# Performance work log

Measured on AMD Instinct MI355X. Metric: run time of the kernel, lower is better.

## Reference

```python
import jax, jax.numpy as jnp
import numpy as np

N, D_IN = 16384, 1024
E, K = 16, 2
D_EMB, H_UNITS, D_HID = 128, 1024, 512


def setup_inputs() -> dict:
    key = jax.random.key(0)
    ks = jax.random.split(key, 10)
    s = lambda fan_in: 1.0 / np.sqrt(fan_in)
    return {
        "x": jax.random.normal(ks[0], (N, D_IN), jnp.float32),
        "Wr": jax.random.normal(ks[1], (D_IN, D_EMB), jnp.float32) * s(D_IN),
        "br": jnp.zeros((D_EMB,), jnp.float32),
        "expert_embeddings": jax.random.normal(ks[2], (E, D_EMB), jnp.float32) * s(D_EMB),
        "W1": jax.random.normal(ks[3], (E, D_IN, H_UNITS), jnp.float32) * s(D_IN),
        "b1": jnp.zeros((E, H_UNITS), jnp.float32),
        "W2": jax.random.normal(ks[4], (E, H_UNITS, H_UNITS // 2), jnp.float32) * s(H_UNITS),
        "b2": jnp.zeros((E, H_UNITS // 2), jnp.float32),
        "W3": jax.random.normal(ks[5], (E, H_UNITS // 2, D_HID), jnp.float32) * s(H_UNITS // 2),
        "b3": jnp.zeros((E, D_HID), jnp.float32),
    }


def reference(x, Wr, br, expert_embeddings, W1, b1, W2, b2, W3, b3):
    # Router: query per token [N, D_EMB]
    q = x @ Wr + br
    # Negative squared L2 distance to each expert embedding -> scores [N, E]
    d2 = jnp.sum(jnp.square(q[:, None, :] - expert_embeddings[None, :, :]), axis=-1)
    scores = -d2
    # Top-k gating (softmax over the k selected scores only)
    top_k_scores, top_k_idx = jax.lax.top_k(scores, K)        # [N, K]
    gates = jax.nn.softmax(top_k_scores, axis=-1)             # [N, K]
    # Dense all-expert MLP (as the original: every expert on every token)
    h1 = jax.nn.relu(jnp.einsum('nd,edh->enh', x, W1) + b1[:, None, :])   # [E,N,1024]
    h2 = jax.nn.relu(jnp.einsum('enh,ehm->enm', h1, W2) + b2[:, None, :]) # [E,N,512]
    eo = jnp.einsum('enm,emo->eno', h2, W3) + b3[:, None, :]              # [E,N,D_HID]
    eo_t = jnp.transpose(eo, (1, 0, 2))                                   # [N,E,D_HID]
    # Gather top-k expert outputs per token and combine with gates
    sel = jnp.take_along_axis(eo_t, top_k_idx[:, :, None], axis=1)        # [N,K,D_HID]
    combined = jnp.sum(sel * gates[:, :, None], axis=1)                   # [N,D_HID]
    return combined
```

## Files before the change

### kernel.cpp

```cpp
#include <hip/hip_runtime.h>

typedef unsigned short u16;
typedef __attribute__((ext_vector_type(8))) short short8;
typedef __attribute__((ext_vector_type(4))) float f32x4;

#define N_TOK 16384
#define DIN   1024
#define NE    16
#define DEMB  128
#define H1N   1024
#define H2N   512
#define DOUT  512
#define CAP   34816
#define MT    (CAP/128)
#define RBLK  1024

#define OFF_P      0ul
#define OFF_C      65536ul
#define OFF_CTRL   65792ul
#define OFF_E01    66048ul
#define OFF_G01    197120ul
#define OFF_GTOK   328192ul
#define OFF_GGATE  467456ul
#define OFF_TSLOT  606720ul
#define OFF_BH     737792ul
#define OFF_BB     803328ul
#define OFF_W1T    868864ul
#define OFF_W2T    34423296ul
#define OFF_W3T    51200512ul
#define OFF_XBF    59589120ul
#define OFF_H1     93143552ul
#define OFF_H2     164446720ul
#define OFF_EO     OFF_H1

__device__ __forceinline__ u16 f2bf(float f) {
  union { float f; unsigned u; } v; v.f = f;
  unsigned r = v.u + 0x7fff + ((v.u >> 16) & 1);
  return (u16)(r >> 16);
}

__device__ __forceinline__ void async_copy16(const u16* g, u16* l) {
  __builtin_amdgcn_global_load_lds((const __attribute__((address_space(1))) unsigned*)g,
                                   (__attribute__((address_space(3))) unsigned*)l,
                                   16, 0, 0);
}

__global__ void router_prep(const float* __restrict__ Wr, const float* __restrict__ br,
                            const float* __restrict__ emb, float* __restrict__ P,
                            float* __restrict__ c) {
  int idx = blockIdx.x * 256 + threadIdx.x;
  int row = idx >> 4, e = idx & 15;
  float s = 0.f;
  for (int j = 0; j < DEMB; ++j) s += Wr[row * DEMB + j] * emb[e * DEMB + j];
  P[row * NE + e] = 2.f * s;
  if (idx < NE) {
    float cc = 0.f, n2 = 0.f;
    for (int j = 0; j < DEMB; ++j) {
      float ev = emb[idx * DEMB + j];
      cc += br[j] * ev;
      n2 += ev * ev;
    }
    c[idx] = 2.f * cc - n2;
  }
}

__global__ void __launch_bounds__(256) router_score(
    const float* __restrict__ x, const float* __restrict__ P,
    const float* __restrict__ c, int* __restrict__ e01,
    float* __restrict__ g01, int* __restrict__ bhist,
    u16* __restrict__ xbf) {
  __shared__ float xs[16384];
  __shared__ int lh[16];
  int wave = threadIdx.x >> 6, lane = threadIdx.x & 63;
  int e2 = lane & 7, kgl = lane >> 3;
  int tbase = blockIdx.x * 16 + wave * 4;
  float* xw = xs + wave * 4096;

  if (threadIdx.x < 16) lh[threadIdx.x] = 0;

  u16* xbrow = xbf + (size_t)tbase * DIN;
  #pragma unroll
  for (int t = 0; t < 4; ++t) {
    const float* src = x + (size_t)(tbase + t) * DIN;
    #pragma unroll
    for (int q = 0; q < 4; ++q) {
      int g = q * 256 + lane * 4;
      float4 v = *(const float4*)(src + g);
      *(float4*)(xw + t * 1024 + g) = v;
      ushort4 o;
      o.x = f2bf(v.x); o.y = f2bf(v.y); o.z = f2bf(v.z); o.w = f2bf(v.w);
      *(ushort4*)(xbrow + t * DIN + g) = o;
    }
  }
  __syncthreads();

  int te0 = 2 * e2, te1 = te0 + 1;
  float ce0 = c[te0], ce1 = c[te1];
  const float* Pb = P + te0;

  float acc0[4] = {0.f, 0.f, 0.f, 0.f};
  float acc1[4] = {0.f, 0.f, 0.f, 0.f};
  int cbase = kgl * 128;
  #pragma unroll 4
  for (int i = 0; i < 32; ++i) {
    int w = (kgl * 4 + i * 4) & 127;
    int idx = cbase + w;
    float2 pv0 = *(const float2*)(Pb + (size_t)(idx + 0) * NE);
    float2 pv1 = *(const float2*)(Pb + (size_t)(idx + 1) * NE);
    float2 pv2 = *(const float2*)(Pb + (size_t)(idx + 2) * NE);
    float2 pv3 = *(const float2*)(Pb + (size_t)(idx + 3) * NE);
    #pragma unroll
    for (int t = 0; t < 4; ++t) {
      float4 xv = *(const float4*)(xw + t * 1024 + idx);
      acc0[t] = fmaf(xv.x, pv0.x, acc0[t]); acc1[t] = fmaf(xv.x, pv0.y, acc1[t]);
      acc0[t] = fmaf(xv.y, pv1.x, acc0[t]); acc1[t] = fmaf(xv.y, pv1.y, acc1[t]);
      acc0[t] = fmaf(xv.z, pv2.x, acc0[t]); acc1[t] = fmaf(xv.z, pv2.y, acc1[t]);
      acc0[t] = fmaf(xv.w, pv3.x, acc0[t]); acc1[t] = fmaf(xv.w, pv3.y, acc1[t]);
    }
  }

  for (int t = 0; t < 4; ++t) {
    float s0 = acc0[t], s1 = acc1[t];
    #pragma unroll
    for (int off = 8; off <= 32; off <<= 1) {
      s0 += __shfl_xor(s0, off);
      s1 += __shfl_xor(s1, off);
    }
    s0 += ce0; s1 += ce1;
    float hi; int hidx;
    if (s0 >= s1) { hi = s0; hidx = te0; } else { hi = s1; hidx = te1; }
    float m1 = hi; int i1 = hidx;
    #pragma unroll
    for (int off = 1; off < 8; off <<= 1) {
      float so = __shfl_xor(m1, off); int io = __shfl_xor(i1, off);
      if (so > m1 || (so == m1 && io < i1)) { m1 = so; i1 = io; }
    }
    float c2; int c2i;
    if (i1 == te0)      { c2 = s1; c2i = te1; }
    else if (i1 == te1) { c2 = s0; c2i = te0; }
    else                { c2 = hi; c2i = hidx; }
    float m2 = c2; int i2 = c2i;
    #pragma unroll
    for (int off = 1; off < 8; off <<= 1) {
      float so = __shfl_xor(m2, off); int io = __shfl_xor(i2, off);
      if (so > m2 || (so == m2 && io < i2)) { m2 = so; i2 = io; }
    }
    if (lane == 0) {
      int tok = tbase + t;
      float ev = expf(m2 - m1);
      float inv = 1.f / (1.f + ev);
      e01[tok * 2 + 0] = i1; e01[tok * 2 + 1] = i2;
      g01[tok * 2 + 0] = inv; g01[tok * 2 + 1] = ev * inv;
      atomicAdd(&lh[i1], 1);
      atomicAdd(&lh[i2], 1);
    }
  }
  __syncthreads();
  if (threadIdx.x < 16) bhist[blockIdx.x * 16 + threadIdx.x] = lh[threadIdx.x];
}

__global__ void __launch_bounds__(1024) scan_offsets(
    const int* __restrict__ bhist, int* __restrict__ counts,
    int* __restrict__ poff, int* __restrict__ bbase, int* __restrict__ gtok) {
  int t = threadIdx.x;
  int e = t & 15, ch = t >> 4;
  int b0 = ch * 16;
  int s = 0;
  #pragma unroll
  for (int i = 0; i < 16; ++i) s += bhist[(b0 + i) * 16 + e];
  __shared__ int part[64][16];
  __shared__ int chbase[64][16];
  __shared__ int cnt[16];
  __shared__ int pof[16];
  part[ch][e] = s;
  __syncthreads();
  if (t < 16) {
    int run = 0;
    for (int c2 = 0; c2 < 64; ++c2) { chbase[c2][t] = run; run += part[c2][t]; }
    cnt[t] = run;
  }
  __syncthreads();
  if (t == 0) {
    int off = 0;
    for (int e2 = 0; e2 < NE; ++e2) {
      pof[e2] = off;
      poff[e2] = off;
      counts[e2] = cnt[e2];
      off += (cnt[e2] + 127) & ~127;
    }
    poff[NE] = off;
  }
  __syncthreads();
  int padc = ((cnt[e] + 127) & ~127) - cnt[e];
  int pbase = pof[e] + cnt[e];
  if (ch < padc) gtok[pbase + ch] = 0;
  if (ch + 64 < padc) gtok[pbase + ch + 64] = 0;

  int run = pof[e] + chbase[ch][e];
  #pragma unroll
  for (int i = 0; i < 16; ++i) {
    bbase[(b0 + i) * 16 + e] = run;
    run += bhist[(b0 + i) * 16 + e];
  }
}

__global__ void build_lists(const int* __restrict__ e01, const float* __restrict__ g01,
                            const int* __restrict__ bbase, int* __restrict__ gtok,
                            float* __restrict__ ggate, int* __restrict__ tslot) {
  __shared__ int pos[16];
  int tid = threadIdx.x;
  if (tid < 16) pos[tid] = bbase[blockIdx.x * 16 + tid];
  __syncthreads();
  if (tid < 16) {
    int t = blockIdx.x * 16 + tid;
    #pragma unroll
    for (int k = 0; k < 2; ++k) {
      int e = e01[t * 2 + k];
      int p = atomicAdd(&pos[e], 1);
      gtok[p] = t;
      ggate[p] = g01[t * 2 + k];
      tslot[t * 2 + k] = p;
    }
  }
}

template<int K, int N>
__global__ void conv_w(const float* __restrict__ W, u16* __restrict__ WT) {
  __shared__ float tile[64][65];
  int e = blockIdx.z;
  int n0 = blockIdx.x * 64, k0 = blockIdx.y * 64;
  int tx = threadIdx.x & 63, ty = threadIdx.x >> 6;
  const float* Wb = W + (size_t)e * K * N;
  #pragma unroll
  for (int p = 0; p < 16; ++p) {
    int k = p * 4 + ty;
    tile[k][tx] = Wb[(size_t)(k0 + k) * N + n0 + tx];
  }
  __syncthreads();
  u16* WTb = WT + (size_t)e * N * K;
  #pragma unroll
  for (int p = 0; p < 16; ++p) {
    int n = p * 4 + ty;
    WTb[(size_t)(n0 + n) * K + k0 + tx] = f2bf(tile[tx][n]);
  }
}

template<int MODE, bool INDIR>
__global__ void __launch_bounds__(256)
gemm_moe(const u16* __restrict__ A, const u16* __restrict__ Ball,
         const float* __restrict__ bias, u16* __restrict__ Cb, float* __restrict__ outF,
         const int* __restrict__ poff, const int* __restrict__ counts,
         const int* __restrict__ gtok, const float* __restrict__ ggate,
         int K, int N, int nblk) {
  __shared__ u16 Asm[2][4096];
  __shared__ u16 Bsm[2][4096];

  int bid = blockIdx.x;
  int q = nblk >> 3, r = nblk & 7;
  int xcd = bid & 7, sidx = bid >> 3;
  int wg = (xcd < r ? xcd * (q + 1) : r * (q + 1) + (xcd - r) * q) + sidx;
  int NB = N >> 7;
  int rb = wg / NB, nb = wg - rb * NB;

  int row_base = rb * 128;
  if (row_base >= poff[NE]) return;
  int e = 0;
  while (row_base >= poff[e + 1]) ++e;

  int tid = threadIdx.x;
  int wave = tid >> 6, lane = tid & 63;
  int wm = wave >> 1, wn = wave & 1;
  int fr = lane & 15, kq = lane >> 4;
  int n_base = nb * 128;

  const u16* Brow = Ball + (size_t)e * N * K + (size_t)n_base * K;

  int rr0 = tid >> 2, rr1 = rr0 + 64;
  int ch8 = ((tid & 3) ^ ((rr0 >> 1) & 3)) * 8;
  const u16 *a0, *a1;
  if constexpr (INDIR) {
    a0 = A + (size_t)gtok[row_base + rr0] * K;
    a1 = A + (size_t)gtok[row_base + rr1] * K;
  } else {
    a0 = A + (size_t)(row_base + rr0) * K;
    a1 = A + (size_t)(row_base + rr1) * K;
  }
  const u16* b0 = Brow + (size_t)rr0 * K;
  const u16* b1 = Brow + (size_t)rr1 * K;

  f32x4 acc[4][4];
  #pragma unroll
  for (int m = 0; m < 4; ++m)
    #pragma unroll
    for (int n = 0; n < 4; ++n)
      acc[m][n] = (f32x4){0.f, 0.f, 0.f, 0.f};

  int swz = (fr >> 1) & 3;

  auto stage_tile = [&](int buf, int kt) {
    async_copy16(a0 + kt + ch8, &Asm[buf][tid * 8]);
    async_copy16(a1 + kt + ch8, &Asm[buf][(256 + tid) * 8]);
    async_copy16(b0 + kt + ch8, &Bsm[buf][tid * 8]);
    async_copy16(b1 + kt + ch8, &Bsm[buf][(256 + tid) * 8]);
  };

  stage_tile(0, 0);
  __syncthreads();

  int nstep = K >> 5;
  int cur = 0;
  for (int s = 0; s < nstep; ++s) {
    if (s + 1 < nstep) stage_tile(cur ^ 1, (s + 1) << 5);
    short8 av[4], bv[4];
    #pragma unroll
    for (int m = 0; m < 4; ++m)
      av[m] = *(const short8*)(&Asm[cur][((wm * 64 + m * 16 + fr) * 4 + (kq ^ swz)) * 8]);
    #pragma unroll
    for (int n = 0; n < 4; ++n)
      bv[n] = *(const short8*)(&Bsm[cur][((wn * 64 + n * 16 + fr) * 4 + (kq ^ swz)) * 8]);
    #pragma unroll
    for (int m = 0; m < 4; ++m)
      #pragma unroll
      for (int n = 0; n < 4; ++n)
        acc[m][n] = __builtin_amdgcn_mfma_f32_16x16x32_bf16(av[m], bv[n], acc[m][n], 0, 0, 0);
    __syncthreads();
    cur ^= 1;
  }

  int crow = (lane >> 4) * 4;
  int ccol = lane & 15;
  const float* be = bias + (size_t)e * N;
  if constexpr (MODE == 0) {
    #pragma unroll
    for (int m = 0; m < 4; ++m) {
      int gr0 = row_base + wm * 64 + m * 16 + crow;
      #pragma unroll
      for (int n = 0; n < 4; ++n) {
        int gc = n_base + wn * 64 + n * 16 + ccol;
        float bvs = be[gc];
        #pragma unroll
        for (int r2 = 0; r2 < 4; ++r2) {
          float v = acc[m][n][r2] + bvs;
          v = v > 0.f ? v : 0.f;
          Cb[(size_t)(gr0 + r2) * N + gc] = f2bf(v);
        }
      }
    }
  } else {
    #pragma unroll
    for (int m = 0; m < 4; ++m) {
      int gr0 = row_base + wm * 64 + m * 16 + crow;
      #pragma unroll
      for (int n = 0; n < 4; ++n) {
        int gc = n_base + wn * 64 + n * 16 + ccol;
        float bvs = be[gc];
        #pragma unroll
        for (int r2 = 0; r2 < 4; ++r2)
          outF[(size_t)(gr0 + r2) * N + gc] = acc[m][n][r2] + bvs;
      }
    }
  }
}

__global__ void __launch_bounds__(256) combine_out(
    const float* __restrict__ eo, const int* __restrict__ tslot,
    const float* __restrict__ g01, float* __restrict__ out) {
  int wave = threadIdx.x >> 6, lane = threadIdx.x & 63;
  int tok = blockIdx.x * 4 + wave;
  int s0 = tslot[tok * 2 + 0], s1 = tslot[tok * 2 + 1];
  float g0 = g01[tok * 2 + 0], g1 = g01[tok * 2 + 1];
  const float* r0 = eo + (size_t)s0 * DOUT + lane * 8;
  const float* r1 = eo + (size_t)s1 * DOUT + lane * 8;
  float* o = out + (size_t)tok * DOUT + lane * 8;
  #pragma unroll
  for (int j = 0; j < 2; ++j) {
    float4 v0 = ((const float4*)r0)[j];
    float4 v1 = ((const float4*)r1)[j];
    float4 ov;
    ov.x = g0 * v0.x + g1 * v1.x;
    ov.y = g0 * v0.y + g1 * v1.y;
    ov.z = g0 * v0.z + g1 * v1.z;
    ov.w = g0 * v0.w + g1 * v1.w;
    ((float4*)o)[j] = ov;
  }
}

extern "C" void kernel_launch(void* const* d_in, const int* in_sizes, int n_in,
                              void* d_out, int out_size, void* d_ws, size_t ws_size,
                              hipStream_t stream) {
  const float* x   = (const float*)d_in[0];
  const float* Wr  = (const float*)d_in[1];
  const float* br  = (const float*)d_in[2];
  const float* emb = (const float*)d_in[3];
  const float* W1  = (const float*)d_in[4];
  const float* b1  = (const float*)d_in[5];
  const float* W2  = (const float*)d_in[6];
  const float* b2  = (const float*)d_in[7];
  const float* W3  = (const float*)d_in[8];
  const float* b3  = (const float*)d_in[9];
  float* out = (float*)d_out;
  char* ws = (char*)d_ws;

  float* P      = (float*)(ws + OFF_P);
  float* c      = (float*)(ws + OFF_C);
  int*   counts = (int*)(ws + OFF_CTRL);
  int*   poff   = (int*)(ws + OFF_CTRL + 128);
  int*   e01    = (int*)(ws + OFF_E01);
  float* g01    = (float*)(ws + OFF_G01);
  int*   gtok   = (int*)(ws + OFF_GTOK);
  float* ggate  = (float*)(ws + OFF_GGATE);
  int*   tslot  = (int*)(ws + OFF_TSLOT);
  int*   bhist  = (int*)(ws + OFF_BH);
  int*   bbase  = (int*)(ws + OFF_BB);
  u16*   W1T    = (u16*)(ws + OFF_W1T);
  u16*   W2T    = (u16*)(ws + OFF_W2T);
  u16*   W3T    = (u16*)(ws + OFF_W3T);
  u16*   xbf    = (u16*)(ws + OFF_XBF);
  u16*   h1     = (u16*)(ws + OFF_H1);
  u16*   h2     = (u16*)(ws + OFF_H2);
  float* eo     = (float*)(ws + OFF_EO);

  conv_w<DIN, H1N><<<dim3(H1N / 64, DIN / 64, NE), 256, 0, stream>>>(W1, W1T);
  conv_w<H1N, H2N><<<dim3(H2N / 64, H1N / 64, NE), 256, 0, stream>>>(W2, W2T);
  conv_w<H2N, DOUT><<<dim3(DOUT / 64, H2N / 64, NE), 256, 0, stream>>>(W3, W3T);

  router_prep<<<64, 256, 0, stream>>>(Wr, br, emb, P, c);
  router_score<<<RBLK, 256, 0, stream>>>(x, P, c, e01, g01, bhist, xbf);
  scan_offsets<<<1, 1024, 0, stream>>>(bhist, counts, poff, bbase, gtok);
  build_lists<<<RBLK, 64, 0, stream>>>(e01, g01, bbase, gtok, ggate, tslot);

  int nb1 = (H1N / 128) * MT;
  int nb2 = (H2N / 128) * MT;
  int nb3 = (DOUT / 128) * MT;
  gemm_moe<0, true><<<nb1, 256, 0, stream>>>(xbf, W1T, b1, h1, nullptr,
                                             poff, counts, gtok, nullptr, DIN, H1N, nb1);
  gemm_moe<0, false><<<nb2, 256, 0, stream>>>(h1, W2T, b2, h2, nullptr,
                                              poff, counts, nullptr, nullptr, H1N, H2N, nb2);
  gemm_moe<2, false><<<nb3, 256, 0, stream>>>(h2, W3T, b3, nullptr, eo,
                                              poff, counts, nullptr, nullptr, H2N, DOUT, nb3);
  combine_out<<<N_TOK / 4, 256, 0, stream>>>(eo, tslot, g01, out);
}
```

Baseline: 291.8 us.

## Use two waves per 128x128 GEMM tile with 64x128 per-wave subtiles

The grouped MoE GEMM drops from four waves to two per workgroup, keeping the 128x128 output tile, so each wave now computes a 64x128 subtile with 32 accumulators. Each wave does more MFMAs per LDS fragment read, which raises register-level reuse and halves the barrier participants. The cost is about twice the accumulator registers, so occupancy and latency hiding may drop, and each thread now issues twice as many async copies per stage.

Result: slower. 321.7 us (+10.3%).

```diff
diff --git a/kernel.cpp b/kernel.cpp
--- a/kernel.cpp
+++ b/kernel.cpp
@@ -246,7 +246,7 @@
 }
 
 template<int MODE, bool INDIR>
-__global__ void __launch_bounds__(256)
+__global__ void __launch_bounds__(128, 2)
 gemm_moe(const u16* __restrict__ A, const u16* __restrict__ Ball,
          const float* __restrict__ bias, u16* __restrict__ Cb, float* __restrict__ outF,
          const int* __restrict__ poff, const int* __restrict__ counts,
@@ -268,40 +268,38 @@
   while (row_base >= poff[e + 1]) ++e;
 
   int tid = threadIdx.x;
-  int wave = tid >> 6, lane = tid & 63;
-  int wm = wave >> 1, wn = wave & 1;
+  int wv = tid >> 6, lane = tid & 63;
   int fr = lane & 15, kq = lane >> 4;
   int n_base = nb * 128;
 
   const u16* Brow = Ball + (size_t)e * N * K + (size_t)n_base * K;
 
-  int rr0 = tid >> 2, rr1 = rr0 + 64;
-  int ch8 = ((tid & 3) ^ ((rr0 >> 1) & 3)) * 8;
-  const u16 *a0, *a1;
-  if constexpr (INDIR) {
-    a0 = A + (size_t)gtok[row_base + rr0] * K;
-    a1 = A + (size_t)gtok[row_base + rr1] * K;
-  } else {
-    a0 = A + (size_t)(row_base + rr0) * K;
-    a1 = A + (size_t)(row_base + rr1) * K;
-  }
-  const u16* b0 = Brow + (size_t)rr0 * K;
-  const u16* b1 = Brow + (size_t)rr1 * K;
-
-  f32x4 acc[4][4];
+  int r0 = tid >> 2;
+  int ch8 = ((tid & 3) ^ ((r0 >> 1) & 3)) * 8;
+  const u16 *ap[4], *bp[4];
+  #pragma unroll
+  for (int j = 0; j < 4; ++j) {
+    int rr = r0 + 32 * j;
+    if constexpr (INDIR) ap[j] = A + (size_t)gtok[row_base + rr] * K;
+    else                 ap[j] = A + (size_t)(row_base + rr) * K;
+    bp[j] = Brow + (size_t)rr * K;
+  }
+
+  f32x4 acc[4][8];
   #pragma unroll
   for (int m = 0; m < 4; ++m)
     #pragma unroll
-    for (int n = 0; n < 4; ++n)
+    for (int n = 0; n < 8; ++n)
       acc[m][n] = (f32x4){0.f, 0.f, 0.f, 0.f};
 
   int swz = (fr >> 1) & 3;
 
   auto stage_tile = [&](int buf, int kt) {
-    async_copy16(a0 + kt + ch8, &Asm[buf][tid * 8]);
-    async_copy16(a1 + kt + ch8, &Asm[buf][(256 + tid) * 8]);
-    async_copy16(b0 + kt + ch8, &Bsm[buf][tid * 8]);
-    async_copy16(b1 + kt + ch8, &Bsm[buf][(256 + tid) * 8]);
+    #pragma unroll
+    for (int j = 0; j < 4; ++j) {
+      async_copy16(ap[j] + kt + ch8, &Asm[buf][(j * 128 + tid) * 8]);
+      async_copy16(bp[j] + kt + ch8, &Bsm[buf][(j * 128 + tid) * 8]);
+    }
   };
 
   stage_tile(0, 0);
@@ -311,52 +309,41 @@
   int cur = 0;
   for (int s = 0; s < nstep; ++s) {
     if (s + 1 < nstep) stage_tile(cur ^ 1, (s + 1) << 5);
-    short8 av[4], bv[4];
+    short8 av[4], bv[8];
     #pragma unroll
     for (int m = 0; m < 4; ++m)
-      av[m] = *(const short8*)(&Asm[cur][((wm * 64 + m * 16 + fr) * 4 + (kq ^ swz)) * 8]);
-    #pragma unroll
-    for (int n = 0; n < 4; ++n)
-      bv[n] = *(const short8*)(&Bsm[cur][((wn * 64 + n * 16 + fr) * 4 + (kq ^ swz)) * 8]);
+      av[m] = *(const short8*)(&Asm[cur][((wv * 64 + m * 16 + fr) * 4 + (kq ^ swz)) * 8]);
+    #pragma unroll
+    for (int n = 0; n < 8; ++n)
+      bv[n] = *(const short8*)(&Bsm[cur][((n * 16 + fr) * 4 + (kq ^ swz)) * 8]);
     #pragma unroll
     for (int m = 0; m < 4; ++m)
       #pragma unroll
-      for (int n = 0; n < 4; ++n)
+      for (int n = 0; n < 8; ++n)
         acc[m][n] = __builtin_amdgcn_mfma_f32_16x16x32_bf16(av[m], bv[n], acc[m][n], 0, 0, 0);
     __syncthreads();
     cur ^= 1;
   }
 
-  int crow = (lane >> 4) * 4;
-  int ccol = lane & 15;
+  int crow = kq * 4;
+  int ccol = fr;
   const float* be = bias + (size_t)e * N;
-  if constexpr (MODE == 0) {
-    #pragma unroll
-    for (int m = 0; m < 4; ++m) {
-      int gr0 = row_base + wm * 64 + m * 16 + crow;
+  #pragma unroll
+  for (int m = 0; m < 4; ++m) {
+    int gr0 = row_base + wv * 64 + m * 16 + crow;
+    #pragma unroll
+    for (int n = 0; n < 8; ++n) {
+      int gc = n_base + n * 16 + ccol;
+      float bvs = be[gc];
       #pragma unroll
-      for (int n = 0; n < 4; ++n) {
-        int gc = n_base + wn * 64 + n * 16 + ccol;
-        float bvs = be[gc];
-        #pragma unroll
-        for (int r2 = 0; r2 < 4; ++r2) {
+      for (int r2 = 0; r2 < 4; ++r2) {
+        if constexpr (MODE == 0) {
           float v = acc[m][n][r2] + bvs;
           v = v > 0.f ? v : 0.f;
           Cb[(size_t)(gr0 + r2) * N + gc] = f2bf(v);
+        } else {
+          outF[(size_t)(gr0 + r2) * N + gc] = acc[m][n][r2] + bvs;
         }
-      }
-    }
-  } else {
-    #pragma unroll
-    for (int m = 0; m < 4; ++m) {
-      int gr0 = row_base + wm * 64 + m * 16 + crow;
-      #pragma unroll
-      for (int n = 0; n < 4; ++n) {
-        int gc = n_base + wn * 64 + n * 16 + ccol;
-        float bvs = be[gc];
-        #pragma unroll
-        for (int r2 = 0; r2 < 4; ++r2)
-          outF[(size_t)(gr0 + r2) * N + gc] = acc[m][n][r2] + bvs;
       }
     }
   }
@@ -432,11 +419,11 @@
   int nb1 = (H1N / 128) * MT;
   int nb2 = (H2N / 128) * MT;
   int nb3 = (DOUT / 128) * MT;
-  gemm_moe<0, true><<<nb1, 256, 0, stream>>>(xbf, W1T, b1, h1, nullptr,
+  gemm_moe<0, true><<<nb1, 128, 0, stream>>>(xbf, W1T, b1, h1, nullptr,
                                              poff, counts, gtok, nullptr, DIN, H1N, nb1);
-  gemm_moe<0, false><<<nb2, 256, 0, stream>>>(h1, W2T, b2, h2, nullptr,
+  gemm_moe<0, false><<<nb2, 128, 0, stream>>>(h1, W2T, b2, h2, nullptr,
                                               poff, counts, nullptr, nullptr, H1N, H2N, nb2);
-  gemm_moe<2, false><<<nb3, 256, 0, stream>>>(h2, W3T, b3, nullptr, eo,
+  gemm_moe<2, false><<<nb3, 128, 0, stream>>>(h2, W3T, b3, nullptr, eo,
                                               poff, counts, nullptr, nullptr, H2N, DOUT, nb3);
   combine_out<<<N_TOK / 4, 256, 0, stream>>>(eo, tslot, g01, out);
 }
```
